# Optimization experiments

Hardware: AMD Instinct MI355X
Metric: run time of the kernel (lower is better)

The kernel has to match this reference:

```python
import jax, jax.numpy as jnp
import numpy as np

B, N, F = 1024, 64, 512
EPS = 1e-8
NEG = -1e12


def setup_inputs() -> dict:
    key = jax.random.key(0)
    k1, k2, k3, k4, k5 = jax.random.split(key, 5)
    h = jax.random.normal(k1, (B, N, F), dtype=jnp.float32)
    # Linear weights stored as (in, out); math identical to torch x @ W.T
    W_h = jax.random.normal(k2, (F, F), dtype=jnp.float32) / np.sqrt(F)
    A_w1 = jax.random.normal(k3, (N, 4 * N), dtype=jnp.float32) / np.sqrt(N)
    A_w2 = jax.random.normal(k4, (4 * N, N), dtype=jnp.float32) / np.sqrt(4 * N)
    beta = jax.random.uniform(k5, (1,), dtype=jnp.float32)
    return {"h": h, "W_h": W_h, "beta": beta, "A_w1": A_w1, "A_w2": A_w2}


def _pearson_corr(x):
    # x: [B, N, F] -> pairwise Pearson correlation over feature dim: [B, N, N]
    xm = x - jnp.mean(x, axis=-1, keepdims=True)
    cov = jnp.einsum('bnf,bmf->bnm', xm, xm)          # [B, N, N]
    norm = jnp.sqrt(jnp.sum(xm * xm, axis=-1))        # [B, N]
    denom = norm[:, :, None] * norm[:, None, :] + EPS
    return cov / denom


def reference(h, W_h, beta, A_w1, A_w2):
    Wh = jnp.einsum('bnf,fg->bng', h, W_h)            # [B, N, F]
    corr_p = _pearson_corr(Wh)                        # [B, N, N]
    e = beta * jnp.abs(corr_p)                        # [B, N, N]
    # Adaptive graph structure learning: small MLP on last (node) dim
    hidden = jax.nn.relu(jnp.einsum('bnm,mk->bnk', e, A_w1))
    adj = jax.nn.relu(e + jnp.einsum('bnk,km->bnm', hidden, A_w2))
    attention = jnp.where(adj > 0, e, NEG)
    attention = jax.nn.softmax(attention, axis=-1)
    # dropout is identity in eval/reference mode
    h_prime = jnp.einsum('bnm,bmf->bnf', attention, Wh)
    return h_prime
```

## Files before the change

kernel.cpp:

```cpp
#include <hip/hip_runtime.h>
#include <math.h>

#define B_ 1024
#define N_ 64
#define F_ 512

typedef const __attribute__((address_space(1))) float* gptr_t;
typedef __attribute__((address_space(3))) float* lptr_t;
typedef _Float16 half_t;
typedef half_t half8 __attribute__((ext_vector_type(8)));
typedef half_t half4 __attribute__((ext_vector_type(4)));
typedef float f32x4 __attribute__((ext_vector_type(4)));

__device__ __forceinline__ void gload16(const float* g, float* l) {
  __builtin_amdgcn_global_load_lds((gptr_t)g, (lptr_t)l, 16, 0, 0);
}

#define XMI(n, f) ((n) * 128 + (((((f) >> 3) ^ ((n) >> 0 & 7))) << 3) + ((f) & 7))
#define SQI(n, m) ((n) * 64 + (((((m) >> 3) ^ ((n) & 7))) << 3) + ((m) & 7))

#define MFMA3(accv, ah, al, bh, bl)                                           \
  do {                                                                        \
    accv = __builtin_amdgcn_mfma_f32_16x16x32_f16(ah, bh, accv, 0, 0, 0);     \
    accv = __builtin_amdgcn_mfma_f32_16x16x32_f16(ah, bl, accv, 0, 0, 0);     \
    accv = __builtin_amdgcn_mfma_f32_16x16x32_f16(al, bh, accv, 0, 0, 0);     \
  } while (0)

__global__ __launch_bounds__(256) void k_split_w(const float* __restrict__ W,
                                                 half_t* __restrict__ wt_hi,
                                                 half_t* __restrict__ wt_lo) {
  int idx = blockIdx.x * 256 + threadIdx.x;
  int k = idx >> 9, n = idx & 511;
  float wv = W[idx] * 512.0f;
  half_t hh = (half_t)wv;
  half_t hl = (half_t)(wv - (float)hh);
  int f = (n ^ (n >> 1)) & 3;
  int pos = ((k >> 3) & 3) ^ f;
  int addr = n * 512 + (k & ~31) + (pos << 3) + (k & 7);
  wt_hi[addr] = hh;
  wt_lo[addr] = hl;
}

__global__ __launch_bounds__(256, 3) void k_wh(const float* __restrict__ hA,
                                               const half_t* __restrict__ WTh,
                                               const half_t* __restrict__ WTl,
                                               float* __restrict__ Wh) {
  __shared__ half_t Ah[128 * 32];
  __shared__ half_t Alo[128 * 32];
  __shared__ half_t Bh[2][128 * 32];
  __shared__ half_t Bl[2][128 * 32];

  const int bid = blockIdx.x;
  const int wg  = (bid & 7) * 256 + (bid >> 3);
  const int mt  = wg >> 2;
  const int nt  = wg & 3;
  const int t = threadIdx.x;
  const int w = t >> 6, lane = t & 63;
  const int wr = w >> 1, wc = w & 1;
  const int lr = lane & 15, ko = lane >> 4;

  const float* Ab = hA + (size_t)mt * 128 * F_;
  const int n0 = nt * 128;

  int Arow[2], Aoct[2], Aad[2];
#pragma unroll
  for (int i = 0; i < 2; ++i) {
    int id = t + 256 * i;
    int row = id >> 2, oct = id & 3;
    Arow[i] = row;
    Aoct[i] = oct;
    Aad[i] = row * 32 + ((oct ^ ((row ^ (row >> 1)) & 3)) << 3);
  }
  int Bsrc[2], Blds[2];
#pragma unroll
  for (int i = 0; i < 2; ++i) {
    int s = t + 256 * i;
    int n = s >> 2, sl = s & 3;
    Bsrc[i] = (n0 + n) * 512 + sl * 8;
    Blds[i] = s * 8;
  }

  f32x4 acc[4][4];
#pragma unroll
  for (int i = 0; i < 4; ++i)
#pragma unroll
    for (int j = 0; j < 4; ++j) acc[i][j] = (f32x4){0.f, 0.f, 0.f, 0.f};

  float4 areg[2][2];

#define LOADA(k0)                                                            \
  do {                                                                       \
    _Pragma("unroll") for (int i_ = 0; i_ < 2; ++i_) {                       \
      const float* p = Ab + (size_t)Arow[i_] * F_ + (k0) + Aoct[i_] * 8;     \
      areg[i_][0] = *(const float4*)p;                                       \
      areg[i_][1] = *(const float4*)(p + 4);                                 \
    }                                                                        \
  } while (0)

#define WRITEA()                                                             \
  do {                                                                       \
    _Pragma("unroll") for (int i_ = 0; i_ < 2; ++i_) {                       \
      half8 hh, hl;                                                          \
      _Pragma("unroll") for (int q = 0; q < 4; ++q) {                        \
        float xs = ((const float*)&areg[i_][0])[q] * 16.0f;                  \
        half_t h = (half_t)xs;                                               \
        hh[q] = h; hl[q] = (half_t)(xs - (float)h);                          \
      }                                                                      \
      _Pragma("unroll") for (int q = 0; q < 4; ++q) {                        \
        float xs = ((const float*)&areg[i_][1])[q] * 16.0f;                  \
        half_t h = (half_t)xs;                                               \
        hh[4 + q] = h; hl[4 + q] = (half_t)(xs - (float)h);                  \
      }                                                                      \
      *(half8*)&Ah[Aad[i_]] = hh;                                            \
      *(half8*)&Alo[Aad[i_]] = hl;                                           \
    }                                                                        \
  } while (0)

#define STAGE_B(buf, k0)                                                     \
  do {                                                                       \
    _Pragma("unroll") for (int i_ = 0; i_ < 2; ++i_)                         \
        gload16((const float*)(WTh + (size_t)(k0) + Bsrc[i_]),               \
                (float*)&Bh[buf][Blds[i_]]);                                 \
    _Pragma("unroll") for (int i_ = 0; i_ < 2; ++i_)                         \
        gload16((const float*)(WTl + (size_t)(k0) + Bsrc[i_]),               \
                (float*)&Bl[buf][Blds[i_]]);                                 \
  } while (0)

  LOADA(0);
  STAGE_B(0, 0);
  WRITEA();
  __syncthreads();

#pragma unroll 1
  for (int kt = 0; kt < 16; ++kt) {
    const int cur = kt & 1;
    if (kt < 15) {
      LOADA((kt + 1) * 32);
      STAGE_B(cur ^ 1, (kt + 1) * 32);
    }

    half8 ah[4], al[4];
#pragma unroll
    for (int i = 0; i < 4; ++i) {
      int r = wr * 64 + i * 16 + lr;
      int pa = r * 32 + ((ko ^ ((r ^ (r >> 1)) & 3)) << 3);
      ah[i] = *(const half8*)&Ah[pa];
      al[i] = *(const half8*)&Alo[pa];
    }

    if (kt < 15)
      asm volatile("s_waitcnt lgkmcnt(0) vmcnt(8)" ::: "memory");
    else
      asm volatile("s_waitcnt lgkmcnt(0) vmcnt(0)" ::: "memory");
    __builtin_amdgcn_sched_barrier(0);
    __builtin_amdgcn_s_barrier();
    __builtin_amdgcn_sched_barrier(0);

    if (kt < 15) WRITEA();

    __builtin_amdgcn_s_setprio(1);
#pragma unroll
    for (int j = 0; j < 4; ++j) {
      int nb = wc * 64 + j * 16 + lr;
      int p = ko ^ ((nb ^ (nb >> 1)) & 3);
      half8 bh = *(const half8*)&Bh[cur][nb * 32 + p * 8];
      half8 bl = *(const half8*)&Bl[cur][nb * 32 + p * 8];
#pragma unroll
      for (int i = 0; i < 4; ++i) MFMA3(acc[i][j], ah[i], al[i], bh, bl);
    }
    __builtin_amdgcn_s_setprio(0);

    asm volatile("s_waitcnt lgkmcnt(0)" ::: "memory");
    __builtin_amdgcn_sched_barrier(0);
    __builtin_amdgcn_s_barrier();
    __builtin_amdgcn_sched_barrier(0);
  }

  const float sc = 1.0f / 8192.0f;
  float* whb = Wh + ((size_t)mt * 128 + wr * 64) * F_ + n0 + wc * 64;
#pragma unroll
  for (int i = 0; i < 4; ++i) {
#pragma unroll
    for (int rr = 0; rr < 4; ++rr) {
      int row = i * 16 + ko * 4 + rr;
#pragma unroll
      for (int j = 0; j < 4; ++j)
        whb[row * F_ + j * 16 + lr] = acc[i][j][rr] * sc;
    }
  }
#undef LOADA
#undef WRITEA
#undef STAGE_B
}

__global__ __launch_bounds__(256) void k_attn(const float* __restrict__ Wh,
                                              const float* __restrict__ A1,
                                              const float* __restrict__ A2,
                                              const float* __restrict__ betap,
                                              float* __restrict__ out) {
  __shared__ float sm[12416];
  half_t* e_h   = (half_t*)sm;
  half_t* e_l   = e_h + 4096;
  half_t* xm_h  = (half_t*)(sm + 4096);
  half_t* xm_l  = xm_h + 8192;
  half_t* hid_h = (half_t*)(sm + 4096);
  half_t* hid_l = (half_t*)(sm + 6144);
  half_t* ab_h  = (half_t*)(sm + 8192);
  half_t* ab_l  = (half_t*)(sm + 10240);
  half_t* at_h  = (half_t*)sm;
  half_t* at_l  = at_h + 4096;
  half_t* wt_h  = (half_t*)(sm + 4096);
  half_t* wt_l  = (half_t*)(sm + 8192);
  float* mu  = sm + 12288;
  float* nrm = sm + 12352;

  const int b = blockIdx.x;
  const int t = threadIdx.x;
  const int w = t >> 6, lane = t & 63;
  const int lr = lane & 15, ko = lane >> 4;
  const float beta = betap[0];
  const float* whb = Wh + (size_t)b * N_ * F_;

  float4 vbuf[8];
#define LOAD_XM(c_)                                                           \
  do {                                                                        \
    _Pragma("unroll") for (int i_ = 0; i_ < 8; ++i_) {                        \
      int id_ = t + 256 * i_;                                                 \
      int n_ = id_ >> 5, c4_ = id_ & 31;                                      \
      vbuf[i_] = *(const float4*)(whb + n_ * F_ + (c_) * 128 + c4_ * 4);      \
    }                                                                         \
  } while (0)

  if (t < 64) mu[t] = 0.f;
  LOAD_XM(0);
  __syncthreads();

  f32x4 covA[4];
#pragma unroll
  for (int j = 0; j < 4; ++j) covA[j] = (f32x4){0.f, 0.f, 0.f, 0.f};

#pragma unroll 1
  for (int c = 0; c < 4; ++c) {
#pragma unroll
    for (int i = 0; i < 8; ++i) {
      int id = t + 256 * i;
      int n = id >> 5, c4 = id & 31;
      float4 v = vbuf[i];
      float s4 = v.x + v.y + v.z + v.w;
      float x0 = v.x * 16.f, x1 = v.y * 16.f;
      float x2 = v.z * 16.f, x3 = v.w * 16.f;
      half4 hh, hl;
      hh[0] = (half_t)x0; hl[0] = (half_t)(x0 - (float)hh[0]);
      hh[1] = (half_t)x1; hl[1] = (half_t)(x1 - (float)hh[1]);
      hh[2] = (half_t)x2; hl[2] = (half_t)(x2 - (float)hh[2]);
      hh[3] = (half_t)x3; hl[3] = (half_t)(x3 - (float)hh[3]);
      int ad = n * 128 + (((c4 >> 1) ^ (n & 7)) << 3) + (c4 & 1) * 4;
      *(half4*)&xm_h[ad] = hh;
      *(half4*)&xm_l[ad] = hl;
      s4 += __shfl_xor(s4, 1);
      s4 += __shfl_xor(s4, 2);
      s4 += __shfl_xor(s4, 4);
      s4 += __shfl_xor(s4, 8);
      s4 += __shfl_xor(s4, 16);
      if ((lane & 31) == 0) mu[n] += s4;
    }
    __syncthreads();
    if (c < 3) LOAD_XM(c + 1);
#pragma unroll
    for (int s = 0; s < 4; ++s) {
      int ra = w * 16 + lr;
      half8 ah = *(const half8*)&xm_h[XMI(ra, (s * 4 + ko) * 8)];
      half8 al = *(const half8*)&xm_l[XMI(ra, (s * 4 + ko) * 8)];
#pragma unroll
      for (int j = 0; j < 4; ++j) {
        int rb = j * 16 + lr;
        half8 bh = *(const half8*)&xm_h[XMI(rb, (s * 4 + ko) * 8)];
        half8 bl = *(const half8*)&xm_l[XMI(rb, (s * 4 + ko) * 8)];
        covA[j] = __builtin_amdgcn_mfma_f32_16x16x32_f16(ah, bh, covA[j], 0, 0, 0);
        covA[j] = __builtin_amdgcn_mfma_f32_16x16x32_f16(ah, bl, covA[j], 0, 0, 0);
        covA[j] = __builtin_amdgcn_mfma_f32_16x16x32_f16(al, bh, covA[j], 0, 0, 0);
      }
    }
    __syncthreads();
  }
#undef LOAD_XM

  {
    float sn[4], smv[4];
#pragma unroll
    for (int r = 0; r < 4; ++r) sn[r] = mu[w * 16 + 4 * ko + r];
#pragma unroll
    for (int j = 0; j < 4; ++j) smv[j] = mu[j * 16 + lr];
#pragma unroll
    for (int j = 0; j < 4; ++j)
#pragma unroll
      for (int r = 0; r < 4; ++r) covA[j][r] -= 0.5f * sn[r] * smv[j];
  }
#pragma unroll
  for (int r = 0; r < 4; ++r)
    if (lr == 4 * ko + r) nrm[w * 16 + lr] = sqrtf(fmaxf(covA[w][r], 0.f));
  __syncthreads();

  float e32[4][4];
#pragma unroll
  for (int j = 0; j < 4; ++j) {
#pragma unroll
    for (int r = 0; r < 4; ++r) {
      int n = w * 16 + 4 * ko + r;
      int m = j * 16 + lr;
      float denom = nrm[n] * nrm[m] + 2.56e-6f;
      float e = beta * fabsf(covA[j][r] / denom);
      e32[j][r] = e;
      float es = e * 16.f;
      half_t hh = (half_t)es;
      e_h[SQI(n, m)] = hh;
      e_l[SQI(n, m)] = (half_t)(es - (float)hh);
    }
  }

  float a1buf[16], a2buf[16];
#define LOAD_A1(jc_)                                                          \
  do {                                                                        \
    _Pragma("unroll") for (int hf_ = 0; hf_ < 2; ++hf_)                       \
      _Pragma("unroll") for (int q_ = 0; q_ < 8; ++q_)                        \
        a1buf[hf_ * 8 + q_] =                                                 \
            A1[(size_t)((w + 4 * hf_) * 8 + q_) * 256 + (jc_) * 64 + lane];   \
  } while (0)
#define LOAD_A2(jc_)                                                          \
  do {                                                                        \
    _Pragma("unroll") for (int hf_ = 0; hf_ < 2; ++hf_)                       \
      _Pragma("unroll") for (int q_ = 0; q_ < 8; ++q_)                        \
        a2buf[hf_ * 8 + q_] =                                                 \
            A2[(size_t)((jc_) * 64 + (w + 4 * hf_) * 8 + q_) * 64 + lane];    \
  } while (0)

  LOAD_A1(0);
  __syncthreads();

  f32x4 adj[4];
#pragma unroll
  for (int j = 0; j < 4; ++j) adj[j] = (f32x4){0.f, 0.f, 0.f, 0.f};

#pragma unroll 1
  for (int jc = 0; jc < 4; ++jc) {
#pragma unroll
    for (int hf = 0; hf < 2; ++hf) {
      int mo = w + 4 * hf;
      int jl = lane;
      half8 hh, hl;
#pragma unroll
      for (int q = 0; q < 8; ++q) {
        float x = a1buf[hf * 8 + q] * 64.f;
        half_t h = (half_t)x;
        hh[q] = h; hl[q] = (half_t)(x - (float)h);
      }
      int ad = jl * 64 + ((mo ^ (jl & 7)) << 3);
      *(half8*)&ab_h[ad] = hh;
      *(half8*)&ab_l[ad] = hl;
    }
    __syncthreads();
    LOAD_A2(jc);

    f32x4 h1[4];
#pragma unroll
    for (int j = 0; j < 4; ++j) h1[j] = (f32x4){0.f, 0.f, 0.f, 0.f};
#pragma unroll
    for (int s = 0; s < 2; ++s) {
      int ra = w * 16 + lr;
      half8 ah = *(const half8*)&e_h[SQI(ra, (s * 4 + ko) * 8)];
      half8 al = *(const half8*)&e_l[SQI(ra, (s * 4 + ko) * 8)];
#pragma unroll
      for (int jt = 0; jt < 4; ++jt) {
        int jl = jt * 16 + lr;
        half8 bh = *(const half8*)&ab_h[SQI(jl, (s * 4 + ko) * 8)];
        half8 bl = *(const half8*)&ab_l[SQI(jl, (s * 4 + ko) * 8)];
        h1[jt] = __builtin_amdgcn_mfma_f32_16x16x32_f16(ah, bh, h1[jt], 0, 0, 0);
        h1[jt] = __builtin_amdgcn_mfma_f32_16x16x32_f16(ah, bl, h1[jt], 0, 0, 0);
        h1[jt] = __builtin_amdgcn_mfma_f32_16x16x32_f16(al, bh, h1[jt], 0, 0, 0);
      }
    }
#pragma unroll
    for (int jt = 0; jt < 4; ++jt) {
#pragma unroll
      for (int r = 0; r < 4; ++r) {
        float x = fmaxf(h1[jt][r], 0.f);
        int n = w * 16 + 4 * ko + r;
        int jl = jt * 16 + lr;
        half_t hh = (half_t)x;
        hid_h[SQI(n, jl)] = hh;
        hid_l[SQI(n, jl)] = (half_t)(x - (float)hh);
      }
    }
    __syncthreads();

#pragma unroll
    for (int hf = 0; hf < 2; ++hf) {
      int ko2 = w + 4 * hf;
      int m = lane;
      half8 hh, hl;
#pragma unroll
      for (int q = 0; q < 8; ++q) {
        float x = a2buf[hf * 8 + q] * 64.f;
        half_t h = (half_t)x;
        hh[q] = h; hl[q] = (half_t)(x - (float)h);
      }
      int ad = m * 64 + ((ko2 ^ (m & 7)) << 3);
      *(half8*)&ab_h[ad] = hh;
      *(half8*)&ab_l[ad] = hl;
    }
    __syncthreads();
    if (jc < 3) LOAD_A1(jc + 1);

#pragma unroll
    for (int s = 0; s < 2; ++s) {
      int ra = w * 16 + lr;
      half8 ah = *(const half8*)&hid_h[SQI(ra, (s * 4 + ko) * 8)];
      half8 al = *(const half8*)&hid_l[SQI(ra, (s * 4 + ko) * 8)];
#pragma unroll
      for (int mt = 0; mt < 4; ++mt) {
        int m = mt * 16 + lr;
        half8 bh = *(const half8*)&ab_h[SQI(m, (s * 4 + ko) * 8)];
        half8 bl = *(const half8*)&ab_l[SQI(m, (s * 4 + ko) * 8)];
        adj[mt] = __builtin_amdgcn_mfma_f32_16x16x32_f16(ah, bh, adj[mt], 0, 0, 0);
        adj[mt] = __builtin_amdgcn_mfma_f32_16x16x32_f16(ah, bl, adj[mt], 0, 0, 0);
        adj[mt] = __builtin_amdgcn_mfma_f32_16x16x32_f16(al, bh, adj[mt], 0, 0, 0);
      }
    }
    __syncthreads();
  }
#undef LOAD_A1
#undef LOAD_A2

  {
    float p[4][4];
#pragma unroll
    for (int r = 0; r < 4; ++r) {
      float mx = -3.0e38f;
#pragma unroll
      for (int mt = 0; mt < 4; ++mt) {
        float pre = e32[mt][r] + adj[mt][r] * (1.f / 65536.f);
        p[mt][r] = (pre > 0.f) ? e32[mt][r] : -1e12f;
        mx = fmaxf(mx, p[mt][r]);
      }
      mx = fmaxf(mx, __shfl_xor(mx, 1));
      mx = fmaxf(mx, __shfl_xor(mx, 2));
      mx = fmaxf(mx, __shfl_xor(mx, 4));
      mx = fmaxf(mx, __shfl_xor(mx, 8));
      float ssum = 0.f;
#pragma unroll
      for (int mt = 0; mt < 4; ++mt) {
        p[mt][r] = expf(p[mt][r] - mx);
        ssum += p[mt][r];
      }
      ssum += __shfl_xor(ssum, 1);
      ssum += __shfl_xor(ssum, 2);
      ssum += __shfl_xor(ssum, 4);
      ssum += __shfl_xor(ssum, 8);
      float inv = 1.f / ssum;
      int n = w * 16 + 4 * ko + r;
#pragma unroll
      for (int mt = 0; mt < 4; ++mt) {
        float pv = p[mt][r] * inv;
        int m = mt * 16 + lr;
        half_t hh = (half_t)pv;
        at_h[SQI(n, m)] = hh;
        at_l[SQI(n, m)] = (half_t)(pv - (float)hh);
      }
    }
  }

  const int fl0 = t & 127;
  const int moB = t >> 7;
  float wbuf[32];
#define LOAD_WT(fc_)                                                          \
  do {                                                                        \
    _Pragma("unroll") for (int i_ = 0; i_ < 4; ++i_) {                        \
      int mo_ = moB + 2 * i_;                                                 \
      _Pragma("unroll") for (int q_ = 0; q_ < 8; ++q_)                        \
        wbuf[i_ * 8 + q_] =                                                   \
            whb[(size_t)(mo_ * 8 + q_) * F_ + (fc_) * 128 + fl0];             \
    }                                                                         \
  } while (0)

  LOAD_WT(0);
#pragma unroll 1
  for (int fc = 0; fc < 4; ++fc) {
    __syncthreads();
#pragma unroll
    for (int i = 0; i < 4; ++i) {
      int mo = moB + 2 * i;
      half8 hh, hl;
#pragma unroll
      for (int q = 0; q < 8; ++q) {
        float x = wbuf[i * 8 + q];
        half_t h = (half_t)x;
        hh[q] = h; hl[q] = (half_t)(x - (float)h);
      }
      int ad = fl0 * 64 + ((mo ^ (fl0 & 7)) << 3);
      *(half8*)&wt_h[ad] = hh;
      *(half8*)&wt_l[ad] = hl;
    }
    __syncthreads();
    if (fc < 3) LOAD_WT(fc + 1);

    half8 aah[2], aal[2];
#pragma unroll
    for (int s = 0; s < 2; ++s) {
      int n = w * 16 + lr;
      aah[s] = *(const half8*)&at_h[SQI(n, (s * 4 + ko) * 8)];
      aal[s] = *(const half8*)&at_l[SQI(n, (s * 4 + ko) * 8)];
    }
#pragma unroll
    for (int ft = 0; ft < 8; ++ft) {
      f32x4 po = (f32x4){0.f, 0.f, 0.f, 0.f};
#pragma unroll
      for (int s = 0; s < 2; ++s) {
        int fl = ft * 16 + lr;
        int ad = fl * 64 + (((((s * 4 + ko)) ^ (fl & 7))) << 3);
        half8 bh = *(const half8*)&wt_h[ad];
        half8 bl = *(const half8*)&wt_l[ad];
        po = __builtin_amdgcn_mfma_f32_16x16x32_f16(aah[s], bh, po, 0, 0, 0);
        po = __builtin_amdgcn_mfma_f32_16x16x32_f16(aah[s], bl, po, 0, 0, 0);
        po = __builtin_amdgcn_mfma_f32_16x16x32_f16(aal[s], bh, po, 0, 0, 0);
      }
      int fg = fc * 128 + ft * 16 + lr;
#pragma unroll
      for (int r = 0; r < 4; ++r) {
        int n = w * 16 + 4 * ko + r;
        out[(size_t)b * N_ * F_ + n * F_ + fg] = po[r];
      }
    }
  }
#undef LOAD_WT
}

extern "C" void kernel_launch(void* const* d_in, const int* in_sizes, int n_in,
                              void* d_out, int out_size, void* d_ws, size_t ws_size,
                              hipStream_t stream) {
  const float* h    = (const float*)d_in[0];
  const float* W    = (const float*)d_in[1];
  const float* beta = (const float*)d_in[2];
  const float* A1   = (const float*)d_in[3];
  const float* A2   = (const float*)d_in[4];
  float* out = (float*)d_out;
  float* Wh  = (float*)d_ws;

  half_t* wt_hi = (half_t*)d_out;
  half_t* wt_lo = wt_hi + 512 * 512;

  k_split_w<<<1024, 256, 0, stream>>>(W, wt_hi, wt_lo);
  k_wh<<<2048, 256, 0, stream>>>(h, wt_hi, wt_lo, Wh);
  k_attn<<<B_, 256, 0, stream>>>(Wh, A1, A2, beta, out);
}
```

Baseline: 221.0 us.

## Load GEMM A operand directly into MFMA registers, bypassing LDS staging

The Wh GEMM kernel no longer stages the fp32 A tile through shared memory. Each wave now loads its own rows straight from global memory into the MFMA fragment layout and does the hi/lo fp16 split in registers. This removes the A LDS buffers, the LDS write/read traffic and one of the two block barriers per k-step, and raises the occupancy hint from 3 to 4 blocks. In exchange, A is read from global twice (once per column-wave) with less coalesced 32-byte accesses, and only about one iteration of latency is available to hide those loads.

```diff
diff --git a/kernel.cpp b/kernel.cpp
--- a/kernel.cpp
+++ b/kernel.cpp
@@ -41,12 +41,10 @@
   wt_lo[addr] = hl;
 }
 
-__global__ __launch_bounds__(256, 3) void k_wh(const float* __restrict__ hA,
+__global__ __launch_bounds__(256, 4) void k_wh(const float* __restrict__ hA,
                                                const half_t* __restrict__ WTh,
                                                const half_t* __restrict__ WTl,
                                                float* __restrict__ Wh) {
-  __shared__ half_t Ah[128 * 32];
-  __shared__ half_t Alo[128 * 32];
   __shared__ half_t Bh[2][128 * 32];
   __shared__ half_t Bl[2][128 * 32];
 
@@ -62,15 +60,11 @@
   const float* Ab = hA + (size_t)mt * 128 * F_;
   const int n0 = nt * 128;
 
-  int Arow[2], Aoct[2], Aad[2];
-#pragma unroll
-  for (int i = 0; i < 2; ++i) {
-    int id = t + 256 * i;
-    int row = id >> 2, oct = id & 3;
-    Arow[i] = row;
-    Aoct[i] = oct;
-    Aad[i] = row * 32 + ((oct ^ ((row ^ (row >> 1)) & 3)) << 3);
-  }
+  const float* Arow[4];
+#pragma unroll
+  for (int i = 0; i < 4; ++i)
+    Arow[i] = Ab + (size_t)(wr * 64 + i * 16 + lr) * F_ + ko * 8;
+
   int Bsrc[2], Blds[2];
 #pragma unroll
   for (int i = 0; i < 2; ++i) {
@@ -86,33 +80,13 @@
 #pragma unroll
     for (int j = 0; j < 4; ++j) acc[i][j] = (f32x4){0.f, 0.f, 0.f, 0.f};
 
-  float4 areg[2][2];
+  float4 areg[4][2];
 
 #define LOADA(k0)                                                            \
   do {                                                                       \
-    _Pragma("unroll") for (int i_ = 0; i_ < 2; ++i_) {                       \
-      const float* p = Ab + (size_t)Arow[i_] * F_ + (k0) + Aoct[i_] * 8;     \
-      areg[i_][0] = *(const float4*)p;                                       \
-      areg[i_][1] = *(const float4*)(p + 4);                                 \
-    }                                                                        \
-  } while (0)
-
-#define WRITEA()                                                             \
-  do {                                                                       \
-    _Pragma("unroll") for (int i_ = 0; i_ < 2; ++i_) {                       \
-      half8 hh, hl;                                                          \
-      _Pragma("unroll") for (int q = 0; q < 4; ++q) {                        \
-        float xs = ((const float*)&areg[i_][0])[q] * 16.0f;                  \
-        half_t h = (half_t)xs;                                               \
-        hh[q] = h; hl[q] = (half_t)(xs - (float)h);                          \
-      }                                                                      \
-      _Pragma("unroll") for (int q = 0; q < 4; ++q) {                        \
-        float xs = ((const float*)&areg[i_][1])[q] * 16.0f;                  \
-        half_t h = (half_t)xs;                                               \
-        hh[4 + q] = h; hl[4 + q] = (half_t)(xs - (float)h);                  \
-      }                                                                      \
-      *(half8*)&Ah[Aad[i_]] = hh;                                            \
-      *(half8*)&Alo[Aad[i_]] = hl;                                           \
+    _Pragma("unroll") for (int i_ = 0; i_ < 4; ++i_) {                       \
+      areg[i_][0] = *(const float4*)(Arow[i_] + (k0));                       \
+      areg[i_][1] = *(const float4*)(Arow[i_] + (k0) + 4);                   \
     }                                                                        \
   } while (0)
 
@@ -128,35 +102,39 @@
 
   LOADA(0);
   STAGE_B(0, 0);
-  WRITEA();
   __syncthreads();
 
 #pragma unroll 1
   for (int kt = 0; kt < 16; ++kt) {
     const int cur = kt & 1;
-    if (kt < 15) {
-      LOADA((kt + 1) * 32);
-      STAGE_B(cur ^ 1, (kt + 1) * 32);
-    }
+
+    if (kt > 0) {
+      asm volatile("s_waitcnt vmcnt(8)" ::: "memory");
+      __builtin_amdgcn_sched_barrier(0);
+      __builtin_amdgcn_s_barrier();
+      __builtin_amdgcn_sched_barrier(0);
+    }
+
+    if (kt < 15) STAGE_B(cur ^ 1, (kt + 1) * 32);
 
     half8 ah[4], al[4];
 #pragma unroll
     for (int i = 0; i < 4; ++i) {
-      int r = wr * 64 + i * 16 + lr;
-      int pa = r * 32 + ((ko ^ ((r ^ (r >> 1)) & 3)) << 3);
-      ah[i] = *(const half8*)&Ah[pa];
-      al[i] = *(const half8*)&Alo[pa];
-    }
-
-    if (kt < 15)
-      asm volatile("s_waitcnt lgkmcnt(0) vmcnt(8)" ::: "memory");
-    else
-      asm volatile("s_waitcnt lgkmcnt(0) vmcnt(0)" ::: "memory");
-    __builtin_amdgcn_sched_barrier(0);
-    __builtin_amdgcn_s_barrier();
-    __builtin_amdgcn_sched_barrier(0);
-
-    if (kt < 15) WRITEA();
+#pragma unroll
+      for (int q = 0; q < 4; ++q) {
+        float xs = ((const float*)&areg[i][0])[q] * 16.0f;
+        half_t h = (half_t)xs;
+        ah[i][q] = h;
+        al[i][q] = (half_t)(xs - (float)h);
+      }
+#pragma unroll
+      for (int q = 0; q < 4; ++q) {
+        float xs = ((const float*)&areg[i][1])[q] * 16.0f;
+        half_t h = (half_t)xs;
+        ah[i][4 + q] = h;
+        al[i][4 + q] = (half_t)(xs - (float)h);
+      }
+    }
 
     __builtin_amdgcn_s_setprio(1);
 #pragma unroll
@@ -170,10 +148,7 @@
     }
     __builtin_amdgcn_s_setprio(0);
 
-    asm volatile("s_waitcnt lgkmcnt(0)" ::: "memory");
-    __builtin_amdgcn_sched_barrier(0);
-    __builtin_amdgcn_s_barrier();
-    __builtin_amdgcn_sched_barrier(0);
+    if (kt < 15) LOADA((kt + 1) * 32);
   }
 
   const float sc = 1.0f / 8192.0f;
@@ -189,7 +164,6 @@
     }
   }
 #undef LOADA
-#undef WRITEA
 #undef STAGE_B
 }
 
```

New measurement: 523.0 us. 2.37x slower.
